# Optimization experiments

Hardware: AMD Instinct MI355X
Metric: run time of the kernel (lower is better)

Reference implementation:

```python
import jax, jax.numpy as jnp
import numpy as np
import math

B = 64
N = 2048
EMBED_DIM = 128
N_HEADS = 8
VAL_DIM = EMBED_DIM // N_HEADS  # 16
KEY_DIM = VAL_DIM               # key_dim defaults to val_dim
CLIP = True
NORM = 1.0 / math.sqrt(KEY_DIM)


def _uniform_param(k, shape):
    # torch init: uniform(-stdv, stdv) with stdv = 1/sqrt(size(-1))
    stdv = 1.0 / math.sqrt(shape[-1])
    return jax.random.uniform(k, shape, jnp.float32, -stdv, stdv)


def setup_inputs() -> dict:
    key = jax.random.key(0)
    ks = jax.random.split(key, 11)
    h = jax.random.normal(ks[0], (B, N, EMBED_DIM), jnp.float32)
    adj_c = jax.random.randint(ks[1], (B, N, N), 0, 2).astype(jnp.float32)
    phone_set = jax.random.randint(ks[2], (B,), 1, N - 1)
    return dict(
        h=h, adj_c=adj_c, phone_set=phone_set,
        Wq_bf=_uniform_param(ks[3], (EMBED_DIM, KEY_DIM)),
        Wk_bf=_uniform_param(ks[4], (EMBED_DIM, KEY_DIM)),
        Wv_bf=_uniform_param(ks[5], (EMBED_DIM, VAL_DIM)),
        Wo_bf=_uniform_param(ks[6], (VAL_DIM, EMBED_DIM)),
        Wq_af=_uniform_param(ks[7], (EMBED_DIM, KEY_DIM)),
        Wk_af=_uniform_param(ks[8], (EMBED_DIM, KEY_DIM)),
        Wv_af=_uniform_param(ks[9], (EMBED_DIM, VAL_DIM)),
        Wo_af=_uniform_param(ks[10], (VAL_DIM, EMBED_DIM)),
    )


def _attend(h, h_phone, adj_row, pos_mask, Wq, Wk, Wv, Wo):
    # h: (B,N,D), h_phone: (B,D), adj_row: (B,N), pos_mask: (B,N) bool
    Q = h_phone @ Wq                              # (B,K)
    K = jnp.einsum('bnd,dk->bnk', h, Wk)          # (B,N,K)
    V = jnp.einsum('bnd,dk->bnk', h, Wv)          # (B,N,V)
    compat = NORM * jnp.einsum('bk,bnk->bn', Q, K)
    if CLIP:
        compat = 10.0 * jnp.tanh(compat)
    valid = pos_mask & (adj_row != 0)
    # masked stable softmax over valid positions; fully-masked rows -> zeros
    mx = jnp.max(jnp.where(valid, compat, -jnp.inf), axis=-1, keepdims=True)
    mx = jnp.where(jnp.isfinite(mx), mx, 0.0)
    e = jnp.where(valid, jnp.exp(compat - mx), 0.0)
    s = jnp.sum(e, axis=-1, keepdims=True)
    attn = (e / jnp.where(s > 0, s, 1.0)) * adj_row   # matches attn * adj slice
    head = jnp.einsum('bn,bnk->bk', attn, V)          # (B,V)
    return head @ Wo                                  # (B,D)


def reference(h, adj_c, phone_set, Wq_bf, Wk_bf, Wv_bf, Wo_bf,
              Wq_af, Wk_af, Wv_af, Wo_af):
    b, n, d = h.shape
    bidx = jnp.arange(b)
    h_phone = h[bidx, phone_set]        # (B,D) single query per graph
    adj_row = adj_c[bidx, phone_set]    # (B,N) adjacency row of phone node
    pos = jnp.arange(n)[None, :]
    mask_bf = pos < phone_set[:, None]   # indices [0, phone)
    mask_af = pos >= phone_set[:, None]  # indices [phone, N)
    g_bf = _attend(h, h_phone, adj_row, mask_bf, Wq_bf, Wk_bf, Wv_bf, Wo_bf)
    g_af = _attend(h, h_phone, adj_row, mask_af, Wq_af, Wk_af, Wv_af, Wo_af)
    return (g_bf, g_af)
```

## Files before the change

### kernel.cpp

```cpp
#include <hip/hip_runtime.h>
#include <math.h>

#define BB 64
#define NN 2048
#define DD 128
#define KD 16
#define NORMF 0.25f
#define CHUNK 32
#define PSTRIDE 260

__device__ __forceinline__ void wave_lds_fence() {
    asm volatile("s_waitcnt lgkmcnt(0)" ::: "memory");
    __builtin_amdgcn_wave_barrier();
}

template <int P>
__global__ __launch_bounds__(256)
void attn_main(const float* __restrict__ h,
               const float* __restrict__ adj,
               const int*   __restrict__ phone,
               const float* __restrict__ Wq_bf, const float* __restrict__ Wk_bf,
               const float* __restrict__ Wq_af, const float* __restrict__ Wk_af,
               float* __restrict__ ws)
{
    constexpr int K = 16 / P;
    const int tid  = threadIdx.x;
    const int wid  = tid >> 6;
    const int lane = tid & 63;
    const int half = lane >> 5;
    const int l    = lane & 31;
    const int dbase = 4 * l;

    const int xcd  = blockIdx.x & 7;
    const int slot = blockIdx.x >> 3;
    const int b    = xcd + 8 * (slot / P);
    const int bip  = slot % P;
    const int ph   = phone[b];

    __shared__ float hp[DD];
    __shared__ float qpart[32][8];
    __shared__ float q[2][KD];
    __shared__ float w_s[2][DD];
    __shared__ float part[4][CHUNK][33];
    __shared__ float ea_s[4][CHUNK];
    __shared__ float red_h[4][2][DD];
    __shared__ float red_s[4][2];

    const float* hb     = h + (size_t)b * NN * DD;
    const float* adjrow = adj + ((size_t)b * NN + ph) * NN;
    const int chbase    = (bip * 4 + wid) * K;

    float adjv[K];
    #pragma unroll
    for (int c = 0; c < K; ++c) adjv[c] = adjrow[(chbase + c) * CHUNK + l];

    if (tid < DD) hp[tid] = hb[(size_t)ph * DD + tid];
    __syncthreads();

    {
        const int pair = tid >> 3, sub = tid & 7;
        const int br = pair >> 4, k = pair & 15;
        const float* Wq = br ? Wq_af : Wq_bf;
        float acc = 0.f;
        #pragma unroll
        for (int i = 0; i < 16; ++i) {
            const int d = sub * 16 + i;
            acc += hp[d] * Wq[d * KD + k];
        }
        qpart[pair][sub] = acc;
    }
    __syncthreads();
    if (tid < 32) {
        float acc = 0.f;
        #pragma unroll
        for (int i = 0; i < 8; ++i) acc += qpart[tid][i];
        q[tid >> 4][tid & 15] = acc;
    }
    __syncthreads();
    {
        const int br = tid >> 7, d = tid & 127;
        const float* Wk = br ? Wk_af : Wk_bf;
        float acc = 0.f;
        #pragma unroll
        for (int k = 0; k < KD; ++k) acc += Wk[d * KD + k] * q[br][k];
        w_s[br][d] = NORMF * acc;
    }
    __syncthreads();

    const float4 wbf = *(const float4*)(&w_s[0][dbase]);
    const float4 waf = *(const float4*)(&w_s[1][dbase]);

    float sbf = 0.f, saf = 0.f;
    float hgbf[4] = {0, 0, 0, 0}, hgaf[4] = {0, 0, 0, 0};

    #pragma unroll
    for (int c = 0; c < K; ++c) {
        const int n0 = (chbase + c) * CHUNK;
        const unsigned long long mask = __ballot(adjv[c] != 0.f);

        float4 hv[16];
        #pragma unroll
        for (int t = 0; t < 16; ++t) {
            const int r = 2 * t + half;
            hv[t] = make_float4(0.f, 0.f, 0.f, 0.f);
            if ((mask >> r) & 1ull)
                hv[t] = *(const float4*)(hb + (size_t)(n0 + r) * DD + dbase);
        }

        #pragma unroll
        for (int t = 0; t < 16; ++t) {
            const int r = 2 * t + half;
            const float4 w = ((n0 + r) >= ph) ? waf : wbf;
            part[wid][r][l] = hv[t].x * w.x + hv[t].y * w.y + hv[t].z * w.z + hv[t].w * w.w;
        }
        wave_lds_fence();

        float a0 = 0.f, a1 = 0.f, a2 = 0.f, a3 = 0.f;
        #pragma unroll
        for (int j = 0; j < 32; j += 4) {
            a0 += part[wid][l][j];
            a1 += part[wid][l][j + 1];
            a2 += part[wid][l][j + 2];
            a3 += part[wid][l][j + 3];
        }
        const float p = (a0 + a1) + (a2 + a3);
        const float e = __expf(10.f * tanhf(p) - 10.f);
        const float es = (adjv[c] != 0.f) ? e : 0.f;
        const float ea = es * adjv[c];
        const bool rowaf = (n0 + l) >= ph;
        sbf += rowaf ? 0.f : es;
        saf += rowaf ? es : 0.f;
        if (lane < 32) ea_s[wid][l] = ea;
        wave_lds_fence();

        #pragma unroll
        for (int t = 0; t < 16; ++t) {
            const int r = 2 * t + half;
            const float ear = ea_s[wid][r];
            const bool af = (n0 + r) >= ph;
            const float eb = af ? 0.f : ear;
            const float ef = af ? ear : 0.f;
            hgbf[0] += eb * hv[t].x; hgbf[1] += eb * hv[t].y;
            hgbf[2] += eb * hv[t].z; hgbf[3] += eb * hv[t].w;
            hgaf[0] += ef * hv[t].x; hgaf[1] += ef * hv[t].y;
            hgaf[2] += ef * hv[t].z; hgaf[3] += ef * hv[t].w;
        }
    }

    #pragma unroll
    for (int m = 1; m <= 16; m <<= 1) {
        sbf += __shfl_xor(sbf, m, 64);
        saf += __shfl_xor(saf, m, 64);
    }
    #pragma unroll
    for (int i = 0; i < 4; ++i) {
        hgbf[i] += __shfl_xor(hgbf[i], 32, 64);
        hgaf[i] += __shfl_xor(hgaf[i], 32, 64);
    }
    if (lane < 32) {
        #pragma unroll
        for (int i = 0; i < 4; ++i) {
            red_h[wid][0][dbase + i] = hgbf[i];
            red_h[wid][1][dbase + i] = hgaf[i];
        }
    }
    if (lane == 0) { red_s[wid][0] = sbf; red_s[wid][1] = saf; }
    __syncthreads();

    {
        const int br = tid >> 7, d = tid & 127;
        float* op = ws + (size_t)(b * P + bip) * PSTRIDE;
        op[br * DD + d] = red_h[0][br][d] + red_h[1][br][d] + red_h[2][br][d] + red_h[3][br][d];
        if (tid < 2)
            op[2 * DD + tid] = red_s[0][tid] + red_s[1][tid] + red_s[2][tid] + red_s[3][tid];
    }
}

template <int P>
__global__ __launch_bounds__(256)
void finalize_kernel(const float* __restrict__ Wv_bf, const float* __restrict__ Wo_bf,
                     const float* __restrict__ Wv_af, const float* __restrict__ Wo_af,
                     const float* __restrict__ ws, float* __restrict__ out)
{
    const int b = blockIdx.x;
    const int tid = threadIdx.x;
    __shared__ float hs[2][DD];
    __shared__ float ssum[2];
    __shared__ float hpart[32][8];
    __shared__ float head[2][KD];

    const int pair = tid >> 3, sub = tid & 7;
    const int brv = pair >> 4, kv = pair & 15;
    const float* Wv = brv ? Wv_af : Wv_bf;
    float wvr[16];
    #pragma unroll
    for (int i = 0; i < 16; ++i) wvr[i] = Wv[(sub * 16 + i) * KD + kv];

    const int br2 = tid >> 7, j = tid & 127;
    const float* Wo = br2 ? Wo_af : Wo_bf;
    float wor[KD];
    #pragma unroll
    for (int k = 0; k < KD; ++k) wor[k] = Wo[k * DD + j];

    const float* base = ws + (size_t)b * P * PSTRIDE;
    {
        float acc = 0.f;
        #pragma unroll
        for (int p = 0; p < P; ++p) acc += base[(size_t)p * PSTRIDE + br2 * DD + j];
        hs[br2][j] = acc;
    }
    if (tid < 2) {
        float acc = 0.f;
        #pragma unroll
        for (int p = 0; p < P; ++p) acc += base[(size_t)p * PSTRIDE + 2 * DD + tid];
        ssum[tid] = acc;
    }
    __syncthreads();

    {
        float acc = 0.f;
        #pragma unroll
        for (int i = 0; i < 16; ++i) acc += hs[brv][sub * 16 + i] * wvr[i];
        hpart[pair][sub] = acc;
    }
    __syncthreads();
    if (tid < 32) {
        float acc = 0.f;
        #pragma unroll
        for (int i = 0; i < 8; ++i) acc += hpart[tid][i];
        head[tid >> 4][tid & 15] = acc;
    }
    __syncthreads();

    {
        const float s = ssum[br2];
        const float inv = (s > 0.f) ? 1.f / s : 0.f;
        float acc = 0.f;
        #pragma unroll
        for (int k = 0; k < KD; ++k) acc += head[br2][k] * wor[k];
        out[br2 * BB * DD + b * DD + j] = acc * inv;
    }
}

extern "C" void kernel_launch(void* const* d_in, const int* in_sizes, int n_in,
                              void* d_out, int out_size, void* d_ws, size_t ws_size,
                              hipStream_t stream) {
    const float* h     = (const float*)d_in[0];
    const float* adj   = (const float*)d_in[1];
    const int*   phone = (const int*)d_in[2];
    const float* Wq_bf = (const float*)d_in[3];
    const float* Wk_bf = (const float*)d_in[4];
    const float* Wv_bf = (const float*)d_in[5];
    const float* Wo_bf = (const float*)d_in[6];
    const float* Wq_af = (const float*)d_in[7];
    const float* Wk_af = (const float*)d_in[8];
    const float* Wv_af = (const float*)d_in[9];
    const float* Wo_af = (const float*)d_in[10];

    float* out = (float*)d_out;
    float* ws  = (float*)d_ws;

    int P = 16;
    while (P > 1 && (size_t)BB * P * PSTRIDE * sizeof(float) > ws_size) P >>= 1;

    switch (P) {
    case 16:
        attn_main<16><<<BB * 16, 256, 0, stream>>>(h, adj, phone, Wq_bf, Wk_bf, Wq_af, Wk_af, ws);
        finalize_kernel<16><<<BB, 256, 0, stream>>>(Wv_bf, Wo_bf, Wv_af, Wo_af, ws, out);
        break;
    case 8:
        attn_main<8><<<BB * 8, 256, 0, stream>>>(h, adj, phone, Wq_bf, Wk_bf, Wq_af, Wk_af, ws);
        finalize_kernel<8><<<BB, 256, 0, stream>>>(Wv_bf, Wo_bf, Wv_af, Wo_af, ws, out);
        break;
    case 4:
        attn_main<4><<<BB * 4, 256, 0, stream>>>(h, adj, phone, Wq_bf, Wk_bf, Wq_af, Wk_af, ws);
        finalize_kernel<4><<<BB, 256, 0, stream>>>(Wv_bf, Wo_bf, Wv_af, Wo_af, ws, out);
        break;
    case 2:
        attn_main<2><<<BB * 2, 256, 0, stream>>>(h, adj, phone, Wq_bf, Wk_bf, Wq_af, Wk_af, ws);
        finalize_kernel<2><<<BB, 256, 0, stream>>>(Wv_bf, Wo_bf, Wv_af, Wo_af, ws, out);
        break;
    default:
        attn_main<1><<<BB, 256, 0, stream>>>(h, adj, phone, Wq_bf, Wk_bf, Wq_af, Wk_af, ws);
        finalize_kernel<1><<<BB, 256, 0, stream>>>(Wv_bf, Wo_bf, Wv_af, Wo_af, ws, out);
        break;
    }
}
```

Measured before the change: 19.17 us.

## Prefetch two h chunks before query setup and halve block split to P=8

Loads the Wq/Wk weights into registers and issues the first two chunks of h row loads before the query/key-projection barriers, so global memory latency overlaps the setup reductions. The chunk loop now processes chunks in pairs with two register buffers. The default split drops from 16 to 8 blocks per batch, giving each block twice as many chunks, and launch bounds request 2 blocks per CU. This trades more register pressure and fewer blocks (less parallelism) for better latency hiding and less per-block setup overhead.

```diff
diff --git a/kernel.cpp b/kernel.cpp
--- a/kernel.cpp
+++ b/kernel.cpp
@@ -15,7 +15,7 @@
 }
 
 template <int P>
-__global__ __launch_bounds__(256)
+__global__ __launch_bounds__(256, 2)
 void attn_main(const float* __restrict__ h,
                const float* __restrict__ adj,
                const int*   __restrict__ phone,
@@ -55,50 +55,21 @@
     for (int c = 0; c < K; ++c) adjv[c] = adjrow[(chbase + c) * CHUNK + l];
 
     if (tid < DD) hp[tid] = hb[(size_t)ph * DD + tid];
-    __syncthreads();
-
-    {
-        const int pair = tid >> 3, sub = tid & 7;
-        const int br = pair >> 4, k = pair & 15;
-        const float* Wq = br ? Wq_af : Wq_bf;
-        float acc = 0.f;
-        #pragma unroll
-        for (int i = 0; i < 16; ++i) {
-            const int d = sub * 16 + i;
-            acc += hp[d] * Wq[d * KD + k];
-        }
-        qpart[pair][sub] = acc;
-    }
-    __syncthreads();
-    if (tid < 32) {
-        float acc = 0.f;
-        #pragma unroll
-        for (int i = 0; i < 8; ++i) acc += qpart[tid][i];
-        q[tid >> 4][tid & 15] = acc;
-    }
-    __syncthreads();
-    {
-        const int br = tid >> 7, d = tid & 127;
-        const float* Wk = br ? Wk_af : Wk_bf;
-        float acc = 0.f;
-        #pragma unroll
-        for (int k = 0; k < KD; ++k) acc += Wk[d * KD + k] * q[br][k];
-        w_s[br][d] = NORMF * acc;
-    }
-    __syncthreads();
-
-    const float4 wbf = *(const float4*)(&w_s[0][dbase]);
-    const float4 waf = *(const float4*)(&w_s[1][dbase]);
-
-    float sbf = 0.f, saf = 0.f;
-    float hgbf[4] = {0, 0, 0, 0}, hgaf[4] = {0, 0, 0, 0};
-
-    #pragma unroll
-    for (int c = 0; c < K; ++c) {
-        const int n0 = (chbase + c) * CHUNK;
-        const unsigned long long mask = __ballot(adjv[c] != 0.f);
-
-        float4 hv[16];
+
+    const int pair = tid >> 3, sub = tid & 7;
+    const int brq = pair >> 4, kq = pair & 15;
+    const float* Wq = brq ? Wq_af : Wq_bf;
+    float wqr[16];
+    #pragma unroll
+    for (int i = 0; i < 16; ++i) wqr[i] = Wq[(sub * 16 + i) * KD + kq];
+
+    const int brw = tid >> 7, dw = tid & 127;
+    const float* Wk = brw ? Wk_af : Wk_bf;
+    float wkr[KD];
+    #pragma unroll
+    for (int k = 0; k < KD; ++k) wkr[k] = Wk[dw * KD + k];
+
+    auto load_chunk = [&](float4* hv, unsigned long long mask, int n0) {
         #pragma unroll
         for (int t = 0; t < 16; ++t) {
             const int r = 2 * t + half;
@@ -106,7 +77,48 @@
             if ((mask >> r) & 1ull)
                 hv[t] = *(const float4*)(hb + (size_t)(n0 + r) * DD + dbase);
         }
-
+    };
+
+    float4 hv0[16], hv1[16];
+    {
+        const unsigned long long m0 = __ballot(adjv[0] != 0.f);
+        load_chunk(hv0, m0, (chbase + 0) * CHUNK);
+        if (K > 1) {
+            const unsigned long long m1 = __ballot(adjv[1] != 0.f);
+            load_chunk(hv1, m1, (chbase + 1) * CHUNK);
+        }
+    }
+
+    __syncthreads();
+    {
+        float acc = 0.f;
+        #pragma unroll
+        for (int i = 0; i < 16; ++i) acc += hp[sub * 16 + i] * wqr[i];
+        qpart[pair][sub] = acc;
+    }
+    __syncthreads();
+    if (tid < 32) {
+        float acc = 0.f;
+        #pragma unroll
+        for (int i = 0; i < 8; ++i) acc += qpart[tid][i];
+        q[tid >> 4][tid & 15] = acc;
+    }
+    __syncthreads();
+    {
+        float acc = 0.f;
+        #pragma unroll
+        for (int k = 0; k < KD; ++k) acc += wkr[k] * q[brw][k];
+        w_s[brw][dw] = NORMF * acc;
+    }
+    __syncthreads();
+
+    const float4 wbf = *(const float4*)(&w_s[0][dbase]);
+    const float4 waf = *(const float4*)(&w_s[1][dbase]);
+
+    float sbf = 0.f, saf = 0.f;
+    float hgbf[4] = {0, 0, 0, 0}, hgaf[4] = {0, 0, 0, 0};
+
+    auto compute_chunk = [&](int n0, const float4* hv, float adjc) {
         #pragma unroll
         for (int t = 0; t < 16; ++t) {
             const int r = 2 * t + half;
@@ -125,8 +137,8 @@
         }
         const float p = (a0 + a1) + (a2 + a3);
         const float e = __expf(10.f * tanhf(p) - 10.f);
-        const float es = (adjv[c] != 0.f) ? e : 0.f;
-        const float ea = es * adjv[c];
+        const float es = (adjc != 0.f) ? e : 0.f;
+        const float ea = es * adjc;
         const bool rowaf = (n0 + l) >= ph;
         sbf += rowaf ? 0.f : es;
         saf += rowaf ? es : 0.f;
@@ -145,6 +157,21 @@
             hgaf[0] += ef * hv[t].x; hgaf[1] += ef * hv[t].y;
             hgaf[2] += ef * hv[t].z; hgaf[3] += ef * hv[t].w;
         }
+    };
+
+    compute_chunk((chbase + 0) * CHUNK, hv0, adjv[0]);
+    if (K > 1) compute_chunk((chbase + 1) * CHUNK, hv1, adjv[1]);
+
+    #pragma unroll
+    for (int cc = 2; cc < K; cc += 2) {
+        const unsigned long long m0 = __ballot(adjv[cc] != 0.f);
+        load_chunk(hv0, m0, (chbase + cc) * CHUNK);
+        if (cc + 1 < K) {
+            const unsigned long long m1 = __ballot(adjv[cc + 1] != 0.f);
+            load_chunk(hv1, m1, (chbase + cc + 1) * CHUNK);
+        }
+        compute_chunk((chbase + cc) * CHUNK, hv0, adjv[cc]);
+        if (cc + 1 < K) compute_chunk((chbase + cc + 1) * CHUNK, hv1, adjv[cc + 1]);
     }
 
     #pragma unroll
@@ -260,14 +287,10 @@
     float* out = (float*)d_out;
     float* ws  = (float*)d_ws;
 
-    int P = 16;
+    int P = 8;
     while (P > 1 && (size_t)BB * P * PSTRIDE * sizeof(float) > ws_size) P >>= 1;
 
     switch (P) {
-    case 16:
-        attn_main<16><<<BB * 16, 256, 0, stream>>>(h, adj, phone, Wq_bf, Wk_bf, Wq_af, Wk_af, ws);
-        finalize_kernel<16><<<BB, 256, 0, stream>>>(Wv_bf, Wo_bf, Wv_af, Wo_af, ws, out);
-        break;
     case 8:
         attn_main<8><<<BB * 8, 256, 0, stream>>>(h, adj, phone, Wq_bf, Wk_bf, Wq_af, Wk_af, ws);
         finalize_kernel<8><<<BB, 256, 0, stream>>>(Wv_bf, Wo_bf, Wv_af, Wo_af, ws, out);
```

Result: faster. 17.51 us (-8.7%).
